# Performance work log

Measured on AMD Instinct MI355X. Metric: run time of the kernel, lower is better.

## Reference

```python
import jax, jax.numpy as jnp
import numpy as np

TREE_DEPTH = 6
NUM_LEAVES = 2 ** TREE_DEPTH  # 64
KSIZE = 3


def _conv2d_same(x, w):
    # x: [N,Cin,H,W], w: [Cout,Cin,kh,kw], stride 1, pad 1 (SAME for k=3)
    return jax.lax.conv_general_dilated(
        x, w, window_strides=(1, 1), padding='SAME',
        dimension_numbers=('NCHW', 'OIHW', 'NCHW'))


def _normalize_split_weight(w_split):
    # Faithful to the torch preprocessing: clamp negatives to 0; if a filter's
    # sum < 0.1, add 0.1/k^2 to every element. (The final divide in the torch
    # code is unassigned, i.e. a no-op.)
    w = jnp.maximum(w_split, 0.0)
    s = jnp.sum(w, axis=(1, 2, 3), keepdims=True)  # per output channel
    return jnp.where(s < 0.1, w + 0.1 / (KSIZE * KSIZE), w)


def setup_inputs() -> dict:
    key = jax.random.key(0)
    k1, k2, k3, k4, k5 = jax.random.split(key, 5)
    N, C, H, W = 4, 32, 512, 512
    x = jax.random.uniform(k1, (N, 1, H, W), dtype=jnp.float32)
    data = jax.random.normal(k2, (N, C, H, W), dtype=jnp.float32)
    w_split = jax.random.normal(k3, (TREE_DEPTH, 1, KSIZE, KSIZE), dtype=jnp.float32)
    w_pred = jax.random.normal(k4, (NUM_LEAVES, C, KSIZE, KSIZE), dtype=jnp.float32)
    b_pred = jax.random.normal(k5, (NUM_LEAVES,), dtype=jnp.float32)
    return {"x": x, "data": data, "w_split": w_split, "w_pred": w_pred, "b_pred": b_pred}


def reference(x, data, w_split, w_pred, b_pred):
    N, _, H, W = x.shape
    w_s = _normalize_split_weight(w_split)

    # Split decisions: sigmoid conv, bit i set if value < 0.6
    value = jax.nn.sigmoid(_conv2d_same(x, w_s))          # [N,D,H,W]
    bits = (value < 0.6).astype(jnp.int32)                # [N,D,H,W]
    powers = (2 ** jnp.arange(TREE_DEPTH - 1, -1, -1)).astype(jnp.int32)
    leaf = jnp.sum(bits * powers[None, :, None, None], axis=1)  # [N,H,W]

    # Prediction conv over leaves
    pred = _conv2d_same(data, w_pred) + b_pred[None, :, None, None]  # [N,L,H,W]

    # y = sum_c pred_c * (1/L + onehot(leaf)_c) = mean-ish term + gather at leaf
    base = jnp.sum(pred, axis=1) / NUM_LEAVES                         # [N,H,W]
    sel = jnp.take_along_axis(pred, leaf[:, None, :, :], axis=1)[:, 0]  # [N,H,W]
    return base + sel
```

## Files before the change

### kernel.cpp

```cpp
#include <hip/hip_runtime.h>

#define HH 512
#define WW 512
#define HWSZ (512 * 512)
#define NCH 32
#define NLF 64
#define WSTRIDE 288
#define WS_WALL_OFF 128
#define THRESH 0.4054651081081644f

__global__ void prep_kernel(const float* __restrict__ w_split,
                            const float* __restrict__ w_pred,
                            const float* __restrict__ b_pred,
                            float* __restrict__ ws) {
  const int tid = threadIdx.x;
  const int blk = blockIdx.x;
  if (blk < 64) {
    if (tid < 288) {
      const int c = tid / 9, t = tid % 9;
      float s = 0.f;
      #pragma unroll 8
      for (int l = 0; l < 64; ++l) s += w_pred[l * 288 + tid];
      s *= (1.0f / 64.0f);
      ws[WS_WALL_OFF + blk * WSTRIDE + t * 32 + c] = w_pred[blk * 288 + tid] + s;
    }
  } else {
    if (tid < 6) {
      float w[9];
      float s = 0.f;
      #pragma unroll
      for (int e = 0; e < 9; ++e) {
        float v = fmaxf(w_split[tid * 9 + e], 0.f);
        w[e] = v;
        s += v;
      }
      const float add = (s < 0.1f) ? (0.1f / 9.0f) : 0.0f;
      #pragma unroll
      for (int e = 0; e < 9; ++e) ws[tid * 9 + e] = w[e] + add;
    }
    if (tid >= 64 && tid < 128) {
      float s = 0.f;
      for (int j = 0; j < 64; ++j) s += b_pred[j];
      ws[64 + (tid - 64)] = b_pred[tid - 64] + s * (1.0f / 64.0f);
    }
  }
}

__device__ __forceinline__ void load6(const float* __restrict__ rowp, int xx0,
                                      int offL, int offR, float lm, float rm,
                                      float w[6]) {
  const float4 c4 = *(const float4*)(rowp + xx0);
  w[0] = rowp[offL] * lm;
  w[1] = c4.x;
  w[2] = c4.y;
  w[3] = c4.z;
  w[4] = c4.w;
  w[5] = rowp[offR] * rm;
}

template <bool SAME>
__device__ __forceinline__ void conv_accum(const float* __restrict__ dbase,
                                           const float* __restrict__ wall,
                                           const int* __restrict__ lf, int yy,
                                           int xx0, int offL, int offR,
                                           float lm, float rm, float4 acc[4]) {
  const float* wl0 = wall + lf[0] * WSTRIDE;
  const float* wl1 = wall + lf[1] * WSTRIDE;
  const float* wl2 = wall + lf[2] * WSTRIDE;
  const float* wl3 = wall + lf[3] * WSTRIDE;
  #pragma unroll 2
  for (int cg = 0; cg < 8; ++cg) {
    const float* ch0 = dbase + cg * 4 * HWSZ;
    #pragma unroll
    for (int dy = 0; dy < 3; ++dy) {
      const int ry = yy + dy - 1;
      if ((unsigned)ry < 512u) {
        const float* r0 = ch0 + ry * 512;
        const float* r1 = r0 + HWSZ;
        const float* r2 = r1 + HWSZ;
        const float* r3 = r2 + HWSZ;
        float a[6], b[6], c[6], d[6];
        load6(r0, xx0, offL, offR, lm, rm, a);
        load6(r1, xx0, offL, offR, lm, rm, b);
        load6(r2, xx0, offL, offR, lm, rm, c);
        load6(r3, xx0, offL, offR, lm, rm, d);
        #pragma unroll
        for (int dx = 0; dx < 3; ++dx) {
          const int woff = (dy * 3 + dx) * 32 + cg * 4;
          const float4 w0 = *(const float4*)(wl0 + woff);
          const float4 w1 = SAME ? w0 : *(const float4*)(wl1 + woff);
          const float4 w2 = SAME ? w0 : *(const float4*)(wl2 + woff);
          const float4 w3 = SAME ? w0 : *(const float4*)(wl3 + woff);
          acc[0].x = fmaf(a[0 + dx], w0.x, acc[0].x);
          acc[0].y = fmaf(b[0 + dx], w0.y, acc[0].y);
          acc[0].z = fmaf(c[0 + dx], w0.z, acc[0].z);
          acc[0].w = fmaf(d[0 + dx], w0.w, acc[0].w);
          acc[1].x = fmaf(a[1 + dx], w1.x, acc[1].x);
          acc[1].y = fmaf(b[1 + dx], w1.y, acc[1].y);
          acc[1].z = fmaf(c[1 + dx], w1.z, acc[1].z);
          acc[1].w = fmaf(d[1 + dx], w1.w, acc[1].w);
          acc[2].x = fmaf(a[2 + dx], w2.x, acc[2].x);
          acc[2].y = fmaf(b[2 + dx], w2.y, acc[2].y);
          acc[2].z = fmaf(c[2 + dx], w2.z, acc[2].z);
          acc[2].w = fmaf(d[2 + dx], w2.w, acc[2].w);
          acc[3].x = fmaf(a[3 + dx], w3.x, acc[3].x);
          acc[3].y = fmaf(b[3 + dx], w3.y, acc[3].y);
          acc[3].z = fmaf(c[3 + dx], w3.z, acc[3].z);
          acc[3].w = fmaf(d[3 + dx], w3.w, acc[3].w);
        }
      }
    }
  }
}

__global__ __launch_bounds__(256, 4) void main_kernel(
    const float* __restrict__ x, const float* __restrict__ data,
    const float* __restrict__ ws, float* __restrict__ out) {
  const int tid = threadIdx.x;
  const int bx = blockIdx.x;
  const int by = blockIdx.y;
  const int n = blockIdx.z;
  const int xx0 = bx * 128 + (tid & 31) * 4;
  const int yy = by * 8 + (tid >> 5);

  const int offL = max(xx0 - 1, 0);
  const int offR = min(xx0 + 4, 511);
  const float lm = (xx0 > 0) ? 1.f : 0.f;
  const float rm = (xx0 < 508) ? 1.f : 0.f;

  const float* xim = x + (size_t)n * HWSZ;
  float xw[3][6];
  #pragma unroll
  for (int dy = 0; dy < 3; ++dy) {
    const int ry = yy + dy - 1;
    if ((unsigned)ry < 512u) {
      load6(xim + ry * 512, xx0, offL, offR, lm, rm, xw[dy]);
    } else {
      #pragma unroll
      for (int j = 0; j < 6; ++j) xw[dy][j] = 0.f;
    }
  }
  int lf[4] = {0, 0, 0, 0};
  #pragma unroll
  for (int f = 0; f < 6; ++f) {
    float v0 = 0.f, v1 = 0.f, v2 = 0.f, v3 = 0.f;
    #pragma unroll
    for (int dy = 0; dy < 3; ++dy) {
      #pragma unroll
      for (int dx = 0; dx < 3; ++dx) {
        const float wv = ws[f * 9 + dy * 3 + dx];
        v0 = fmaf(xw[dy][0 + dx], wv, v0);
        v1 = fmaf(xw[dy][1 + dx], wv, v1);
        v2 = fmaf(xw[dy][2 + dx], wv, v2);
        v3 = fmaf(xw[dy][3 + dx], wv, v3);
      }
    }
    const int bit = 32 >> f;
    if (v0 < THRESH) lf[0] |= bit;
    if (v1 < THRESH) lf[1] |= bit;
    if (v2 < THRESH) lf[2] |= bit;
    if (v3 < THRESH) lf[3] |= bit;
  }

  float4 acc[4];
  #pragma unroll
  for (int p = 0; p < 4; ++p) acc[p] = make_float4(0.f, 0.f, 0.f, 0.f);

  const float* dbase = data + (size_t)n * NCH * HWSZ;
  const bool same = (lf[0] == lf[1]) && (lf[1] == lf[2]) && (lf[2] == lf[3]);
  if (__all((int)same)) {
    conv_accum<true>(dbase, ws + WS_WALL_OFF, lf, yy, xx0, offL, offR, lm, rm, acc);
  } else {
    conv_accum<false>(dbase, ws + WS_WALL_OFF, lf, yy, xx0, offL, offR, lm, rm, acc);
  }

  float4 res;
  res.x = acc[0].x + acc[0].y + acc[0].z + acc[0].w + ws[64 + lf[0]];
  res.y = acc[1].x + acc[1].y + acc[1].z + acc[1].w + ws[64 + lf[1]];
  res.z = acc[2].x + acc[2].y + acc[2].z + acc[2].w + ws[64 + lf[2]];
  res.w = acc[3].x + acc[3].y + acc[3].z + acc[3].w + ws[64 + lf[3]];
  *(float4*)(out + (size_t)n * HWSZ + yy * 512 + xx0) = res;
}

extern "C" void kernel_launch(void* const* d_in, const int* in_sizes, int n_in,
                              void* d_out, int out_size, void* d_ws,
                              size_t ws_size, hipStream_t stream) {
  const float* x = (const float*)d_in[0];
  const float* data = (const float*)d_in[1];
  const float* w_split = (const float*)d_in[2];
  const float* w_pred = (const float*)d_in[3];
  const float* b_pred = (const float*)d_in[4];
  float* out = (float*)d_out;
  float* ws = (float*)d_ws;

  prep_kernel<<<65, 320, 0, stream>>>(w_split, w_pred, b_pred, ws);
  main_kernel<<<dim3(4, 64, 4), 256, 0, stream>>>(x, data, ws, out);
}
```

Measured before the change: 293.5 us.

## Use two pixels per thread with wave shuffles for horizontal halo

Each thread now computes two output pixels instead of four, and blocks cover four rows with one 64-lane wavefront per row. The left and right neighbour columns come from cross-lane shuffles rather than extra global loads, so only edge lanes do a scalar load. The per-wave uniform-leaf fast path is removed, and the launch bounds rise to allow more waves per CU to raise occupancy and latency hiding. In exchange there are more shuffle instructions and less register-level reuse of weights across pixels, and the grid doubles in size.

New measurement: 276.6 us. 1.06x faster.

```diff
diff --git a/kernel.cpp b/kernel.cpp
--- a/kernel.cpp
+++ b/kernel.cpp
@@ -1,10 +1,7 @@
 #include <hip/hip_runtime.h>
 
-#define HH 512
-#define WW 512
 #define HWSZ (512 * 512)
 #define NCH 32
-#define NLF 64
 #define WSTRIDE 288
 #define WS_WALL_OFF 128
 #define THRESH 0.4054651081081644f
@@ -40,146 +37,135 @@
     }
     if (tid >= 64 && tid < 128) {
       float s = 0.f;
+      #pragma unroll 8
       for (int j = 0; j < 64; ++j) s += b_pred[j];
       ws[64 + (tid - 64)] = b_pred[tid - 64] + s * (1.0f / 64.0f);
     }
   }
 }
 
-__device__ __forceinline__ void load6(const float* __restrict__ rowp, int xx0,
-                                      int offL, int offR, float lm, float rm,
-                                      float w[6]) {
-  const float4 c4 = *(const float4*)(rowp + xx0);
-  w[0] = rowp[offL] * lm;
-  w[1] = c4.x;
-  w[2] = c4.y;
-  w[3] = c4.z;
-  w[4] = c4.w;
-  w[5] = rowp[offR] * rm;
-}
+__global__ __launch_bounds__(256, 8) void main_kernel(
+    const float* __restrict__ x, const float* __restrict__ data,
+    const float* __restrict__ ws, float* __restrict__ out) {
+  const int tid = threadIdx.x;
+  const int lane = tid & 63;
+  const int wvid = tid >> 6;
+  const int bx = blockIdx.x;
+  const int by = blockIdx.y;
+  const int n = blockIdx.z;
+  const int xx0 = bx * 128 + lane * 2;
+  const int yy = by * 4 + wvid;
 
-template <bool SAME>
-__device__ __forceinline__ void conv_accum(const float* __restrict__ dbase,
-                                           const float* __restrict__ wall,
-                                           const int* __restrict__ lf, int yy,
-                                           int xx0, int offL, int offR,
-                                           float lm, float rm, float4 acc[4]) {
-  const float* wl0 = wall + lf[0] * WSTRIDE;
-  const float* wl1 = wall + lf[1] * WSTRIDE;
-  const float* wl2 = wall + lf[2] * WSTRIDE;
-  const float* wl3 = wall + lf[3] * WSTRIDE;
-  #pragma unroll 2
+  const bool isL = (lane == 0);
+  const bool isR = (lane == 63);
+  const bool isEdge = isL || isR;
+  const int ecol = isL ? (xx0 - 1) : (xx0 + 2);
+  const int ecolc = min(max(ecol, 0), 511);
+  const float emask = (ecol >= 0 && ecol < 512) ? 1.f : 0.f;
+
+  const float* xim = x + (size_t)n * HWSZ;
+  float xwin[3][4];
+  #pragma unroll
+  for (int dy = 0; dy < 3; ++dy) {
+    const int ry = yy + dy - 1;
+    if ((unsigned)ry < 512u) {
+      const float* rp = xim + ry * 512;
+      const float2 c2 = *(const float2*)(rp + xx0);
+      float ev = 0.f;
+      if (isEdge) ev = rp[ecolc] * emask;
+      float lft = __shfl(c2.y, tid - 1);
+      float rgt = __shfl(c2.x, tid + 1);
+      if (isL) lft = ev;
+      if (isR) rgt = ev;
+      xwin[dy][0] = lft; xwin[dy][1] = c2.x; xwin[dy][2] = c2.y; xwin[dy][3] = rgt;
+    } else {
+      xwin[dy][0] = xwin[dy][1] = xwin[dy][2] = xwin[dy][3] = 0.f;
+    }
+  }
+  int lf0 = 0, lf1 = 0;
+  #pragma unroll
+  for (int f = 0; f < 6; ++f) {
+    float v0 = 0.f, v1 = 0.f;
+    #pragma unroll
+    for (int dy = 0; dy < 3; ++dy) {
+      #pragma unroll
+      for (int dx = 0; dx < 3; ++dx) {
+        const float wv = ws[f * 9 + dy * 3 + dx];
+        v0 = fmaf(xwin[dy][dx], wv, v0);
+        v1 = fmaf(xwin[dy][dx + 1], wv, v1);
+      }
+    }
+    const int bit = 32 >> f;
+    if (v0 < THRESH) lf0 |= bit;
+    if (v1 < THRESH) lf1 |= bit;
+  }
+
+  const float* wall = ws + WS_WALL_OFF;
+  const float* wl0 = wall + lf0 * WSTRIDE;
+  const float* wl1 = wall + lf1 * WSTRIDE;
+  const float* dbase = data + (size_t)n * NCH * HWSZ;
+
+  float4 acc0 = make_float4(0.f, 0.f, 0.f, 0.f);
+  float4 acc1 = make_float4(0.f, 0.f, 0.f, 0.f);
+
+  #pragma unroll 1
   for (int cg = 0; cg < 8; ++cg) {
-    const float* ch0 = dbase + cg * 4 * HWSZ;
+    const float* ch0 = dbase + (size_t)cg * 4 * HWSZ;
     #pragma unroll
     for (int dy = 0; dy < 3; ++dy) {
       const int ry = yy + dy - 1;
       if ((unsigned)ry < 512u) {
         const float* r0 = ch0 + ry * 512;
-        const float* r1 = r0 + HWSZ;
-        const float* r2 = r1 + HWSZ;
-        const float* r3 = r2 + HWSZ;
-        float a[6], b[6], c[6], d[6];
-        load6(r0, xx0, offL, offR, lm, rm, a);
-        load6(r1, xx0, offL, offR, lm, rm, b);
-        load6(r2, xx0, offL, offR, lm, rm, c);
-        load6(r3, xx0, offL, offR, lm, rm, d);
-        #pragma unroll
-        for (int dx = 0; dx < 3; ++dx) {
-          const int woff = (dy * 3 + dx) * 32 + cg * 4;
-          const float4 w0 = *(const float4*)(wl0 + woff);
-          const float4 w1 = SAME ? w0 : *(const float4*)(wl1 + woff);
-          const float4 w2 = SAME ? w0 : *(const float4*)(wl2 + woff);
-          const float4 w3 = SAME ? w0 : *(const float4*)(wl3 + woff);
-          acc[0].x = fmaf(a[0 + dx], w0.x, acc[0].x);
-          acc[0].y = fmaf(b[0 + dx], w0.y, acc[0].y);
-          acc[0].z = fmaf(c[0 + dx], w0.z, acc[0].z);
-          acc[0].w = fmaf(d[0 + dx], w0.w, acc[0].w);
-          acc[1].x = fmaf(a[1 + dx], w1.x, acc[1].x);
-          acc[1].y = fmaf(b[1 + dx], w1.y, acc[1].y);
-          acc[1].z = fmaf(c[1 + dx], w1.z, acc[1].z);
-          acc[1].w = fmaf(d[1 + dx], w1.w, acc[1].w);
-          acc[2].x = fmaf(a[2 + dx], w2.x, acc[2].x);
-          acc[2].y = fmaf(b[2 + dx], w2.y, acc[2].y);
-          acc[2].z = fmaf(c[2 + dx], w2.z, acc[2].z);
-          acc[2].w = fmaf(d[2 + dx], w2.w, acc[2].w);
-          acc[3].x = fmaf(a[3 + dx], w3.x, acc[3].x);
-          acc[3].y = fmaf(b[3 + dx], w3.y, acc[3].y);
-          acc[3].z = fmaf(c[3 + dx], w3.z, acc[3].z);
-          acc[3].w = fmaf(d[3 + dx], w3.w, acc[3].w);
+        const float2 a2 = *(const float2*)(r0 + xx0);
+        const float2 b2 = *(const float2*)(r0 + HWSZ + xx0);
+        const float2 c2 = *(const float2*)(r0 + 2 * HWSZ + xx0);
+        const float2 d2 = *(const float2*)(r0 + 3 * HWSZ + xx0);
+        float ea = 0.f, eb = 0.f, ec = 0.f, ed = 0.f;
+        if (isEdge) {
+          ea = r0[ecolc] * emask;
+          eb = r0[HWSZ + ecolc] * emask;
+          ec = r0[2 * HWSZ + ecolc] * emask;
+          ed = r0[3 * HWSZ + ecolc] * emask;
+        }
+        float la = __shfl(a2.y, tid - 1), ra = __shfl(a2.x, tid + 1);
+        float lb = __shfl(b2.y, tid - 1), rb = __shfl(b2.x, tid + 1);
+        float lc = __shfl(c2.y, tid - 1), rc = __shfl(c2.x, tid + 1);
+        float ld = __shfl(d2.y, tid - 1), rd = __shfl(d2.x, tid + 1);
+        if (isL) { la = ea; lb = eb; lc = ec; ld = ed; }
+        if (isR) { ra = ea; rb = eb; rc = ec; rd = ed; }
+
+        const int tbase = dy * 3 * 32 + cg * 4;
+        {
+          const float4 w0 = *(const float4*)(wl0 + tbase);
+          const float4 w1 = *(const float4*)(wl1 + tbase);
+          acc0.x = fmaf(la, w0.x, acc0.x); acc1.x = fmaf(a2.x, w1.x, acc1.x);
+          acc0.y = fmaf(lb, w0.y, acc0.y); acc1.y = fmaf(b2.x, w1.y, acc1.y);
+          acc0.z = fmaf(lc, w0.z, acc0.z); acc1.z = fmaf(c2.x, w1.z, acc1.z);
+          acc0.w = fmaf(ld, w0.w, acc0.w); acc1.w = fmaf(d2.x, w1.w, acc1.w);
+        }
+        {
+          const float4 w0 = *(const float4*)(wl0 + tbase + 32);
+          const float4 w1 = *(const float4*)(wl1 + tbase + 32);
+          acc0.x = fmaf(a2.x, w0.x, acc0.x); acc1.x = fmaf(a2.y, w1.x, acc1.x);
+          acc0.y = fmaf(b2.x, w0.y, acc0.y); acc1.y = fmaf(b2.y, w1.y, acc1.y);
+          acc0.z = fmaf(c2.x, w0.z, acc0.z); acc1.z = fmaf(c2.y, w1.z, acc1.z);
+          acc0.w = fmaf(d2.x, w0.w, acc0.w); acc1.w = fmaf(d2.y, w1.w, acc1.w);
+        }
+        {
+          const float4 w0 = *(const float4*)(wl0 + tbase + 64);
+          const float4 w1 = *(const float4*)(wl1 + tbase + 64);
+          acc0.x = fmaf(a2.y, w0.x, acc0.x); acc1.x = fmaf(ra, w1.x, acc1.x);
+          acc0.y = fmaf(b2.y, w0.y, acc0.y); acc1.y = fmaf(rb, w1.y, acc1.y);
+          acc0.z = fmaf(c2.y, w0.z, acc0.z); acc1.z = fmaf(rc, w1.z, acc1.z);
+          acc0.w = fmaf(d2.y, w0.w, acc0.w); acc1.w = fmaf(rd, w1.w, acc1.w);
         }
       }
     }
   }
-}
 
-__global__ __launch_bounds__(256, 4) void main_kernel(
-    const float* __restrict__ x, const float* __restrict__ data,
-    const float* __restrict__ ws, float* __restrict__ out) {
-  const int tid = threadIdx.x;
-  const int bx = blockIdx.x;
-  const int by = blockIdx.y;
-  const int n = blockIdx.z;
-  const int xx0 = bx * 128 + (tid & 31) * 4;
-  const int yy = by * 8 + (tid >> 5);
-
-  const int offL = max(xx0 - 1, 0);
-  const int offR = min(xx0 + 4, 511);
-  const float lm = (xx0 > 0) ? 1.f : 0.f;
-  const float rm = (xx0 < 508) ? 1.f : 0.f;
-
-  const float* xim = x + (size_t)n * HWSZ;
-  float xw[3][6];
-  #pragma unroll
-  for (int dy = 0; dy < 3; ++dy) {
-    const int ry = yy + dy - 1;
-    if ((unsigned)ry < 512u) {
-      load6(xim + ry * 512, xx0, offL, offR, lm, rm, xw[dy]);
-    } else {
-      #pragma unroll
-      for (int j = 0; j < 6; ++j) xw[dy][j] = 0.f;
-    }
-  }
-  int lf[4] = {0, 0, 0, 0};
-  #pragma unroll
-  for (int f = 0; f < 6; ++f) {
-    float v0 = 0.f, v1 = 0.f, v2 = 0.f, v3 = 0.f;
-    #pragma unroll
-    for (int dy = 0; dy < 3; ++dy) {
-      #pragma unroll
-      for (int dx = 0; dx < 3; ++dx) {
-        const float wv = ws[f * 9 + dy * 3 + dx];
-        v0 = fmaf(xw[dy][0 + dx], wv, v0);
-        v1 = fmaf(xw[dy][1 + dx], wv, v1);
-        v2 = fmaf(xw[dy][2 + dx], wv, v2);
-        v3 = fmaf(xw[dy][3 + dx], wv, v3);
-      }
-    }
-    const int bit = 32 >> f;
-    if (v0 < THRESH) lf[0] |= bit;
-    if (v1 < THRESH) lf[1] |= bit;
-    if (v2 < THRESH) lf[2] |= bit;
-    if (v3 < THRESH) lf[3] |= bit;
-  }
-
-  float4 acc[4];
-  #pragma unroll
-  for (int p = 0; p < 4; ++p) acc[p] = make_float4(0.f, 0.f, 0.f, 0.f);
-
-  const float* dbase = data + (size_t)n * NCH * HWSZ;
-  const bool same = (lf[0] == lf[1]) && (lf[1] == lf[2]) && (lf[2] == lf[3]);
-  if (__all((int)same)) {
-    conv_accum<true>(dbase, ws + WS_WALL_OFF, lf, yy, xx0, offL, offR, lm, rm, acc);
-  } else {
-    conv_accum<false>(dbase, ws + WS_WALL_OFF, lf, yy, xx0, offL, offR, lm, rm, acc);
-  }
-
-  float4 res;
-  res.x = acc[0].x + acc[0].y + acc[0].z + acc[0].w + ws[64 + lf[0]];
-  res.y = acc[1].x + acc[1].y + acc[1].z + acc[1].w + ws[64 + lf[1]];
-  res.z = acc[2].x + acc[2].y + acc[2].z + acc[2].w + ws[64 + lf[2]];
-  res.w = acc[3].x + acc[3].y + acc[3].z + acc[3].w + ws[64 + lf[3]];
-  *(float4*)(out + (size_t)n * HWSZ + yy * 512 + xx0) = res;
+  const float res0 = acc0.x + acc0.y + acc0.z + acc0.w + ws[64 + lf0];
+  const float res1 = acc1.x + acc1.y + acc1.z + acc1.w + ws[64 + lf1];
+  *(float2*)(out + (size_t)n * HWSZ + yy * 512 + xx0) = make_float2(res0, res1);
 }
 
 extern "C" void kernel_launch(void* const* d_in, const int* in_sizes, int n_in,
@@ -194,5 +180,5 @@
   float* ws = (float*)d_ws;
 
   prep_kernel<<<65, 320, 0, stream>>>(w_split, w_pred, b_pred, ws);
-  main_kernel<<<dim3(4, 64, 4), 256, 0, stream>>>(x, data, ws, out);
+  main_kernel<<<dim3(4, 128, 4), 256, 0, stream>>>(x, data, ws, out);
 }
```
